# Optimization experiments

Measured on AMD Instinct MI355X. Metric: run time of the kernel, lower is better.

The kernel has to match this reference:

```python
import jax, jax.numpy as jnp
import numpy as np

OUT, IN = 4096, 4096
NNZ = 838860  # 0.05 * OUT * IN
ALPHA = 1.0   # set_privacy(True)


def setup_inputs() -> dict:
    key = jax.random.key(0)
    k1, k2, k3, k4, k5, k6 = jax.random.split(key, 6)
    x = jax.random.normal(k1, (2, 2048, IN), dtype=jnp.float32)
    # packed uint4 pairs stored as bytes (kept in int32 per spec; values in [0,256))
    base_packed = jax.random.randint(k2, (OUT, IN // 2), 0, 256, dtype=jnp.int32)
    # per-row dequant scales (positive, small, like ceiling/7)
    scales = jax.random.uniform(k3, (OUT, 1), dtype=jnp.float32, minval=1e-3, maxval=5e-2)
    ortho_vals = jax.random.normal(k4, (NNZ,), dtype=jnp.float32) * 0.02
    ortho_rows = jax.random.randint(k5, (NNZ,), 0, OUT, dtype=jnp.int32)
    ortho_cols = jax.random.randint(k6, (NNZ,), 0, IN, dtype=jnp.int32)
    return {"x": x, "base_packed": base_packed, "scales": scales,
            "ortho_vals": ortho_vals, "ortho_rows": ortho_rows, "ortho_cols": ortho_cols}


def _dequant(base_packed, scales):
    # unpack two int4 values per byte: col 2k <- low nibble, col 2k+1 <- high nibble
    p = base_packed.astype(jnp.int32)
    low = p & 0xF
    high = (p >> 4) & 0xF
    O, K = p.shape
    w_int4 = jnp.stack([low, high], axis=-1).reshape(O, 2 * K) - 8  # offset-binary -> [-8, 7]
    return w_int4.astype(jnp.float32) * scales  # [O, I]


def reference(x, base_packed, scales, ortho_vals, ortho_rows, ortho_cols):
    O = base_packed.shape[0]
    I = 2 * base_packed.shape[1]
    w_base = _dequant(base_packed, scales)  # [O, I] fp32
    # sparse outlier residual scattered into dense weight (CSR spmm equivalent)
    w_corr = jnp.zeros((O, I), jnp.float32).at[ortho_rows, ortho_cols].add(ortho_vals)
    w = w_base + ALPHA * w_corr
    x_flat = x.reshape(-1, I).astype(jnp.float32)
    out = x_flat @ w.T  # [N, O]
    return out.reshape(x.shape[:-1] + (O,)).astype(x.dtype)
```

## Files before the change

### kernel.cpp

```cpp
#include <hip/hip_runtime.h>
#include <cstdint>
#include <cstddef>

typedef __bf16 bf16x8 __attribute__((ext_vector_type(8)));
typedef float f32x4 __attribute__((ext_vector_type(4)));
typedef unsigned short ushort8 __attribute__((ext_vector_type(8)));

#define OUT_DIM 4096
#define IN_DIM 4096
#define NT 64


__device__ __forceinline__ unsigned short f2bf(float f) {
  unsigned u = __float_as_uint(f);
  return (unsigned short)((u + 0x7FFFu + ((u >> 16) & 1u)) >> 16);
}

__device__ __forceinline__ void async_copy16(const void* g, void* l) {
  __builtin_amdgcn_global_load_lds(
      (const __attribute__((address_space(1))) unsigned int*)g,
      (__attribute__((address_space(3))) unsigned int*)l, 16, 0, 0);
}


__global__ __launch_bounds__(256) void dequant_kernel(
    const int* __restrict__ packed, const float* __restrict__ scales,
    unsigned short* __restrict__ wb) {
  int idx = blockIdx.x * 256 + threadIdx.x;
  int4 p = reinterpret_cast<const int4*>(packed)[idx];
  float s = scales[idx >> 9];
  ushort8 o;
  o[0] = f2bf((float)((p.x & 15) - 8) * s);
  o[1] = f2bf((float)(((p.x >> 4) & 15) - 8) * s);
  o[2] = f2bf((float)((p.y & 15) - 8) * s);
  o[3] = f2bf((float)(((p.y >> 4) & 15) - 8) * s);
  o[4] = f2bf((float)((p.z & 15) - 8) * s);
  o[5] = f2bf((float)(((p.z >> 4) & 15) - 8) * s);
  o[6] = f2bf((float)((p.w & 15) - 8) * s);
  o[7] = f2bf((float)(((p.w >> 4) & 15) - 8) * s);
  *reinterpret_cast<ushort8*>(&wb[(size_t)idx * 8]) = o;
}

__global__ __launch_bounds__(256) void scatter_bf16_kernel(
    const float* __restrict__ vals, const int* __restrict__ rows,
    const int* __restrict__ cols, unsigned short* __restrict__ wb, int nnz) {
  int i = blockIdx.x * 256 + threadIdx.x;
  if (i >= nnz) return;
  size_t idx = (size_t)rows[i] * IN_DIM + cols[i];
  unsigned int* word = (unsigned int*)(wb + (idx & ~(size_t)1));
  const bool hi = (idx & 1) != 0;
  const float v = vals[i];
  unsigned int old = *word, assumed;
  do {
    assumed = old;
    unsigned short h = hi ? (unsigned short)(assumed >> 16)
                          : (unsigned short)(assumed & 0xFFFFu);
    float f = __uint_as_float((unsigned)h << 16);
    unsigned short nh = f2bf(f + v);
    unsigned int nw = hi ? ((assumed & 0x0000FFFFu) | ((unsigned)nh << 16))
                         : ((assumed & 0xFFFF0000u) | (unsigned)nh);
    old = atomicCAS(word, assumed, nw);
  } while (old != assumed);
}

__global__ __launch_bounds__(256) void cvt_kernel(
    const float* __restrict__ in, unsigned short* __restrict__ out) {
  int i = blockIdx.x * 256 + threadIdx.x;
  float4 a = reinterpret_cast<const float4*>(in)[2 * i];
  float4 b = reinterpret_cast<const float4*>(in)[2 * i + 1];
  ushort8 o;
  o[0] = f2bf(a.x); o[1] = f2bf(a.y); o[2] = f2bf(a.z); o[3] = f2bf(a.w);
  o[4] = f2bf(b.x); o[5] = f2bf(b.y); o[6] = f2bf(b.z); o[7] = f2bf(b.w);
  *reinterpret_cast<ushort8*>(&out[(size_t)i * 8]) = o;
}


#define SB(buf, op, kh) ((((buf) * 4) + ((op) * 2) + (kh)) * 16384)

#define STAGE(buf, op, kh, kt)                                              \
  do {                                                                      \
    const unsigned short* gsrc_ =                                           \
        (op) ? (const unsigned short*)((const char*)gA + dBA) : gA;         \
    const unsigned short* g_ = gsrc_ + (kt) * 64 + (kh) * 32;               \
    unsigned short* l_ =                                                    \
        (unsigned short*)((char*)lds + SB(buf, op, kh)) + wave * 512;       \
    async_copy16(g_, l_);                                                   \
    async_copy16(g_ + 128 * IN_DIM, l_ + 4096);                             \
  } while (0)

#define MFMA_ __builtin_amdgcn_mfma_f32_16x16x32_bf16

#define LDA4(d0, d1, d2, d3, BUF, KS, MH)                                   \
  d0 = *(const bf16x8*)(ldsc + (laneA + SB(BUF, 0, KS) + (MH) * 4096 + 0)); \
  d1 = *(const bf16x8*)(ldsc + (laneA + SB(BUF, 0, KS) + (MH) * 4096 + 1024)); \
  d2 = *(const bf16x8*)(ldsc + (laneA + SB(BUF, 0, KS) + (MH) * 4096 + 2048)); \
  d3 = *(const bf16x8*)(ldsc + (laneA + SB(BUF, 0, KS) + (MH) * 4096 + 3072))

#define LDB4(d0, d1, d2, d3, BUF, KS)                                       \
  d0 = *(const bf16x8*)(ldsc + (laneB + SB(BUF, 1, KS) + 0));               \
  d1 = *(const bf16x8*)(ldsc + (laneB + SB(BUF, 1, KS) + 1024));            \
  d2 = *(const bf16x8*)(ldsc + (laneB + SB(BUF, 1, KS) + 2048));            \
  d3 = *(const bf16x8*)(ldsc + (laneB + SB(BUF, 1, KS) + 3072))

#define MM16(MH, A0, A1, A2, A3, B0, B1, B2, B3)                            \
  acc[(MH) * 4 + 0][0] = MFMA_(A0, B0, acc[(MH) * 4 + 0][0], 0, 0, 0);      \
  acc[(MH) * 4 + 0][1] = MFMA_(A0, B1, acc[(MH) * 4 + 0][1], 0, 0, 0);      \
  acc[(MH) * 4 + 0][2] = MFMA_(A0, B2, acc[(MH) * 4 + 0][2], 0, 0, 0);      \
  acc[(MH) * 4 + 0][3] = MFMA_(A0, B3, acc[(MH) * 4 + 0][3], 0, 0, 0);      \
  acc[(MH) * 4 + 1][0] = MFMA_(A1, B0, acc[(MH) * 4 + 1][0], 0, 0, 0);      \
  acc[(MH) * 4 + 1][1] = MFMA_(A1, B1, acc[(MH) * 4 + 1][1], 0, 0, 0);      \
  acc[(MH) * 4 + 1][2] = MFMA_(A1, B2, acc[(MH) * 4 + 1][2], 0, 0, 0);      \
  acc[(MH) * 4 + 1][3] = MFMA_(A1, B3, acc[(MH) * 4 + 1][3], 0, 0, 0);      \
  acc[(MH) * 4 + 2][0] = MFMA_(A2, B0, acc[(MH) * 4 + 2][0], 0, 0, 0);      \
  acc[(MH) * 4 + 2][1] = MFMA_(A2, B1, acc[(MH) * 4 + 2][1], 0, 0, 0);      \
  acc[(MH) * 4 + 2][2] = MFMA_(A2, B2, acc[(MH) * 4 + 2][2], 0, 0, 0);      \
  acc[(MH) * 4 + 2][3] = MFMA_(A2, B3, acc[(MH) * 4 + 2][3], 0, 0, 0);      \
  acc[(MH) * 4 + 3][0] = MFMA_(A3, B0, acc[(MH) * 4 + 3][0], 0, 0, 0);      \
  acc[(MH) * 4 + 3][1] = MFMA_(A3, B1, acc[(MH) * 4 + 3][1], 0, 0, 0);      \
  acc[(MH) * 4 + 3][2] = MFMA_(A3, B2, acc[(MH) * 4 + 3][2], 0, 0, 0);      \
  acc[(MH) * 4 + 3][3] = MFMA_(A3, B3, acc[(MH) * 4 + 3][3], 0, 0, 0)

#define PHASE8(BUF, KS, MH, STAGEST, DOWAIT)                                \
  do {                                                                      \
    bf16x8 a0_, a1_, a2_, a3_;                                              \
    LDA4(a0_, a1_, a2_, a3_, BUF, KS, MH);                                  \
    LDB4(bB0, bB1, bB2, bB3, BUF, KS);                                      \
    STAGEST;                                                                \
    if (DOWAIT) asm volatile("s_waitcnt vmcnt(8)" ::: "memory");            \
    __builtin_amdgcn_s_barrier();                                           \
    asm volatile("s_waitcnt lgkmcnt(0)" ::: "memory");                      \
    __builtin_amdgcn_s_setprio(1);                                          \
    MM16(MH, a0_, a1_, a2_, a3_, bB0, bB1, bB2, bB3);                       \
    __builtin_amdgcn_s_setprio(0);                                          \
    __builtin_amdgcn_s_barrier();                                           \
  } while (0)

#define PHASE4(BUF, KS, MH, STAGEST, DOWAIT)                                \
  do {                                                                      \
    bf16x8 a0_, a1_, a2_, a3_;                                              \
    LDA4(a0_, a1_, a2_, a3_, BUF, KS, MH);                                  \
    STAGEST;                                                                \
    if (DOWAIT) asm volatile("s_waitcnt vmcnt(8)" ::: "memory");            \
    __builtin_amdgcn_s_barrier();                                           \
    asm volatile("s_waitcnt lgkmcnt(0)" ::: "memory");                      \
    __builtin_amdgcn_s_setprio(1);                                          \
    MM16(MH, a0_, a1_, a2_, a3_, bB0, bB1, bB2, bB3);                       \
    __builtin_amdgcn_s_setprio(0);                                          \
    __builtin_amdgcn_s_barrier();                                           \
  } while (0)

#define MINC(x) ((x) < NT ? (x) : (NT - 1))

#define TILE(BUF, t)                                                        \
  do {                                                                      \
    PHASE8(BUF, 0, 0, STAGE(1 - (BUF), 0, 1, MINC((t) + 1)), 0);            \
    PHASE4(BUF, 0, 1, STAGE(1 - (BUF), 1, 1, MINC((t) + 1)), 1);            \
    PHASE8(BUF, 1, 0, STAGE(BUF, 0, 0, MINC((t) + 2)), 0);                  \
    PHASE4(BUF, 1, 1, STAGE(BUF, 1, 0, MINC((t) + 2)), 1);                  \
  } while (0)

__global__ __launch_bounds__(512, 2) void gemm_kernel(
    const unsigned short* __restrict__ A,
    const unsigned short* __restrict__ B,
    float* __restrict__ C) {
  __shared__ __align__(16) unsigned short lds[65536];
  const char* ldsc = (const char*)lds;

  const int bid = blockIdx.x;
  const int xcd = bid & 7, i_ = bid >> 3;
  const int bm = (xcd >> 1) * 4 + (i_ >> 3);
  const int bn = (xcd & 1) * 8 + (i_ & 7);
  const int m0 = bm * 256, n0 = bn * 256;

  const int tid = threadIdx.x;
  const int wave = tid >> 6, lane = tid & 63;
  const int wm = wave >> 2, wn = wave & 3;
  const int lrow = lane & 15, lk = lane >> 4;

  const int r0 = tid >> 2, s0 = tid & 3;
  const int s0s = s0 ^ ((r0 >> 1) & 3);
  const unsigned short* gA = A + (size_t)(m0 + r0) * IN_DIM + s0s * 8;
  const ptrdiff_t dBA = ((const char*)B - (const char*)A) +
                        (ptrdiff_t)(n0 - m0) * IN_DIM * 2;

  const int lks = lk ^ ((lrow >> 1) & 3);
  const int laneA = (wm * 128 + lrow) * 64 + lks * 16;
  const int laneB = (wn * 64 + lrow) * 64 + lks * 16;

  f32x4 acc[8][4];
#pragma unroll
  for (int mi = 0; mi < 8; ++mi)
#pragma unroll
    for (int ni = 0; ni < 4; ++ni) acc[mi][ni] = (f32x4){0.f, 0.f, 0.f, 0.f};

  bf16x8 bB0, bB1, bB2, bB3;

  STAGE(0, 0, 0, 0); STAGE(0, 1, 0, 0);
  asm volatile("" ::: "memory");
  STAGE(0, 0, 1, 0); STAGE(0, 1, 1, 0);
  asm volatile("" ::: "memory");
  STAGE(1, 0, 0, 1); STAGE(1, 1, 0, 1);
  asm volatile("s_waitcnt vmcnt(8)" ::: "memory");
  __builtin_amdgcn_s_barrier();

#pragma unroll 1
  for (int p = 0; p < NT / 2; ++p) {
    const int te = 2 * p;
    TILE(0, te);
    TILE(1, te + 1);
  }
  asm volatile("s_waitcnt vmcnt(0) lgkmcnt(0)" ::: "memory");

#pragma unroll
  for (int mi = 0; mi < 8; ++mi)
#pragma unroll
    for (int ni = 0; ni < 4; ++ni) {
      int m = m0 + wm * 128 + mi * 16 + lk * 4;
      int n = n0 + wn * 64 + ni * 16 + lrow;
      float* cp = &C[(size_t)m * OUT_DIM + n];
#pragma unroll
      for (int r = 0; r < 4; ++r) cp[(size_t)r * OUT_DIM] = acc[mi][ni][r];
    }
}


extern "C" void kernel_launch(void* const* d_in, const int* in_sizes, int n_in,
                              void* d_out, int out_size, void* d_ws, size_t ws_size,
                              hipStream_t stream) {
  const float* x      = (const float*)d_in[0];
  const int*   packed = (const int*)d_in[1];
  const float* scales = (const float*)d_in[2];
  const float* vals   = (const float*)d_in[3];
  const int*   rows   = (const int*)d_in[4];
  const int*   cols   = (const int*)d_in[5];
  float* out = (float*)d_out;

  const int nnz = in_sizes[3];

  char* ws = (char*)d_ws;
  const size_t MB = 1024 * 1024;
  unsigned short* Wb = (unsigned short*)ws;
  unsigned short* Xb = (unsigned short*)(ws + 32 * MB);

  dequant_kernel<<<8192, 256, 0, stream>>>(packed, scales, Wb);
  scatter_bf16_kernel<<<(nnz + 255) / 256, 256, 0, stream>>>(vals, rows, cols, Wb, nnz);
  cvt_kernel<<<8192, 256, 0, stream>>>(x, Xb);
  gemm_kernel<<<256, 512, 0, stream>>>(Xb, Wb, out);
}
```

Before: 185.1 us.

## Fuse prep kernels, use packed bf16 atomics for scatter, reschedule GEMM pipeline

Merges the weight dequantization and activation conversion into one launch. The CAS-loop scatter becomes a hardware global_atomic_pk_add_bf16, with each value rounded to bf16 before it is added. The GEMM main loop is restructured: each phase now loads both k-halves for a quarter of the A tile, B fragments are loaded once per tile, and the staging/wait schedule uses a single buffer-ahead with vmcnt(2). The atomic changes rounding slightly, since the value is converted to bf16 first, and the new pipeline schedule risks exposed load latency.

```diff
diff --git a/kernel.cpp b/kernel.cpp
--- a/kernel.cpp
+++ b/kernel.cpp
@@ -23,55 +23,47 @@
 }
 
 
-__global__ __launch_bounds__(256) void dequant_kernel(
+__global__ __launch_bounds__(256) void prep_kernel(
     const int* __restrict__ packed, const float* __restrict__ scales,
-    unsigned short* __restrict__ wb) {
-  int idx = blockIdx.x * 256 + threadIdx.x;
-  int4 p = reinterpret_cast<const int4*>(packed)[idx];
-  float s = scales[idx >> 9];
-  ushort8 o;
-  o[0] = f2bf((float)((p.x & 15) - 8) * s);
-  o[1] = f2bf((float)(((p.x >> 4) & 15) - 8) * s);
-  o[2] = f2bf((float)((p.y & 15) - 8) * s);
-  o[3] = f2bf((float)(((p.y >> 4) & 15) - 8) * s);
-  o[4] = f2bf((float)((p.z & 15) - 8) * s);
-  o[5] = f2bf((float)(((p.z >> 4) & 15) - 8) * s);
-  o[6] = f2bf((float)((p.w & 15) - 8) * s);
-  o[7] = f2bf((float)(((p.w >> 4) & 15) - 8) * s);
-  *reinterpret_cast<ushort8*>(&wb[(size_t)idx * 8]) = o;
-}
-
-__global__ __launch_bounds__(256) void scatter_bf16_kernel(
+    unsigned short* __restrict__ wb, const float* __restrict__ x,
+    unsigned short* __restrict__ xb) {
+  int b = blockIdx.x;
+  if (b < 8192) {
+    int idx = b * 256 + threadIdx.x;
+    int4 p = reinterpret_cast<const int4*>(packed)[idx];
+    float s = scales[idx >> 9];
+    ushort8 o;
+    o[0] = f2bf((float)((p.x & 15) - 8) * s);
+    o[1] = f2bf((float)(((p.x >> 4) & 15) - 8) * s);
+    o[2] = f2bf((float)((p.y & 15) - 8) * s);
+    o[3] = f2bf((float)(((p.y >> 4) & 15) - 8) * s);
+    o[4] = f2bf((float)((p.z & 15) - 8) * s);
+    o[5] = f2bf((float)(((p.z >> 4) & 15) - 8) * s);
+    o[6] = f2bf((float)((p.w & 15) - 8) * s);
+    o[7] = f2bf((float)(((p.w >> 4) & 15) - 8) * s);
+    *reinterpret_cast<ushort8*>(&wb[(size_t)idx * 8]) = o;
+  } else {
+    int i = (b - 8192) * 256 + threadIdx.x;
+    float4 a = reinterpret_cast<const float4*>(x)[2 * i];
+    float4 c = reinterpret_cast<const float4*>(x)[2 * i + 1];
+    ushort8 o;
+    o[0] = f2bf(a.x); o[1] = f2bf(a.y); o[2] = f2bf(a.z); o[3] = f2bf(a.w);
+    o[4] = f2bf(c.x); o[5] = f2bf(c.y); o[6] = f2bf(c.z); o[7] = f2bf(c.w);
+    *reinterpret_cast<ushort8*>(&xb[(size_t)i * 8]) = o;
+  }
+}
+
+__global__ __launch_bounds__(256) void scatter_pk_kernel(
     const float* __restrict__ vals, const int* __restrict__ rows,
     const int* __restrict__ cols, unsigned short* __restrict__ wb, int nnz) {
   int i = blockIdx.x * 256 + threadIdx.x;
   if (i >= nnz) return;
   size_t idx = (size_t)rows[i] * IN_DIM + cols[i];
   unsigned int* word = (unsigned int*)(wb + (idx & ~(size_t)1));
-  const bool hi = (idx & 1) != 0;
-  const float v = vals[i];
-  unsigned int old = *word, assumed;
-  do {
-    assumed = old;
-    unsigned short h = hi ? (unsigned short)(assumed >> 16)
-                          : (unsigned short)(assumed & 0xFFFFu);
-    float f = __uint_as_float((unsigned)h << 16);
-    unsigned short nh = f2bf(f + v);
-    unsigned int nw = hi ? ((assumed & 0x0000FFFFu) | ((unsigned)nh << 16))
-                         : ((assumed & 0xFFFF0000u) | (unsigned)nh);
-    old = atomicCAS(word, assumed, nw);
-  } while (old != assumed);
-}
-
-__global__ __launch_bounds__(256) void cvt_kernel(
-    const float* __restrict__ in, unsigned short* __restrict__ out) {
-  int i = blockIdx.x * 256 + threadIdx.x;
-  float4 a = reinterpret_cast<const float4*>(in)[2 * i];
-  float4 b = reinterpret_cast<const float4*>(in)[2 * i + 1];
-  ushort8 o;
-  o[0] = f2bf(a.x); o[1] = f2bf(a.y); o[2] = f2bf(a.z); o[3] = f2bf(a.w);
-  o[4] = f2bf(b.x); o[5] = f2bf(b.y); o[6] = f2bf(b.z); o[7] = f2bf(b.w);
-  *reinterpret_cast<ushort8*>(&out[(size_t)i * 8]) = o;
+  unsigned short h = f2bf(vals[i]);
+  unsigned int data = (idx & 1) ? ((unsigned)h << 16) : (unsigned)h;
+  asm volatile("global_atomic_pk_add_bf16 %0, %1, off"
+               :: "v"(word), "v"(data) : "memory");
 }
 
 
@@ -90,11 +82,11 @@
 
 #define MFMA_ __builtin_amdgcn_mfma_f32_16x16x32_bf16
 
-#define LDA4(d0, d1, d2, d3, BUF, KS, MH)                                   \
-  d0 = *(const bf16x8*)(ldsc + (laneA + SB(BUF, 0, KS) + (MH) * 4096 + 0)); \
-  d1 = *(const bf16x8*)(ldsc + (laneA + SB(BUF, 0, KS) + (MH) * 4096 + 1024)); \
-  d2 = *(const bf16x8*)(ldsc + (laneA + SB(BUF, 0, KS) + (MH) * 4096 + 2048)); \
-  d3 = *(const bf16x8*)(ldsc + (laneA + SB(BUF, 0, KS) + (MH) * 4096 + 3072))
+#define LDAQ(BUF, Q)                                                        \
+  a00 = *(const bf16x8*)(ldsc + (laneA + SB(BUF, 0, 0) + (2*(Q)) * 1024));  \
+  a01 = *(const bf16x8*)(ldsc + (laneA + SB(BUF, 0, 0) + (2*(Q)+1) * 1024));\
+  a10 = *(const bf16x8*)(ldsc + (laneA + SB(BUF, 0, 1) + (2*(Q)) * 1024));  \
+  a11 = *(const bf16x8*)(ldsc + (laneA + SB(BUF, 0, 1) + (2*(Q)+1) * 1024))
 
 #define LDB4(d0, d1, d2, d3, BUF, KS)                                       \
   d0 = *(const bf16x8*)(ldsc + (laneB + SB(BUF, 1, KS) + 0));               \
@@ -102,49 +94,47 @@
   d2 = *(const bf16x8*)(ldsc + (laneB + SB(BUF, 1, KS) + 2048));            \
   d3 = *(const bf16x8*)(ldsc + (laneB + SB(BUF, 1, KS) + 3072))
 
-#define MM16(MH, A0, A1, A2, A3, B0, B1, B2, B3)                            \
-  acc[(MH) * 4 + 0][0] = MFMA_(A0, B0, acc[(MH) * 4 + 0][0], 0, 0, 0);      \
-  acc[(MH) * 4 + 0][1] = MFMA_(A0, B1, acc[(MH) * 4 + 0][1], 0, 0, 0);      \
-  acc[(MH) * 4 + 0][2] = MFMA_(A0, B2, acc[(MH) * 4 + 0][2], 0, 0, 0);      \
-  acc[(MH) * 4 + 0][3] = MFMA_(A0, B3, acc[(MH) * 4 + 0][3], 0, 0, 0);      \
-  acc[(MH) * 4 + 1][0] = MFMA_(A1, B0, acc[(MH) * 4 + 1][0], 0, 0, 0);      \
-  acc[(MH) * 4 + 1][1] = MFMA_(A1, B1, acc[(MH) * 4 + 1][1], 0, 0, 0);      \
-  acc[(MH) * 4 + 1][2] = MFMA_(A1, B2, acc[(MH) * 4 + 1][2], 0, 0, 0);      \
-  acc[(MH) * 4 + 1][3] = MFMA_(A1, B3, acc[(MH) * 4 + 1][3], 0, 0, 0);      \
-  acc[(MH) * 4 + 2][0] = MFMA_(A2, B0, acc[(MH) * 4 + 2][0], 0, 0, 0);      \
-  acc[(MH) * 4 + 2][1] = MFMA_(A2, B1, acc[(MH) * 4 + 2][1], 0, 0, 0);      \
-  acc[(MH) * 4 + 2][2] = MFMA_(A2, B2, acc[(MH) * 4 + 2][2], 0, 0, 0);      \
-  acc[(MH) * 4 + 2][3] = MFMA_(A2, B3, acc[(MH) * 4 + 2][3], 0, 0, 0);      \
-  acc[(MH) * 4 + 3][0] = MFMA_(A3, B0, acc[(MH) * 4 + 3][0], 0, 0, 0);      \
-  acc[(MH) * 4 + 3][1] = MFMA_(A3, B1, acc[(MH) * 4 + 3][1], 0, 0, 0);      \
-  acc[(MH) * 4 + 3][2] = MFMA_(A3, B2, acc[(MH) * 4 + 3][2], 0, 0, 0);      \
-  acc[(MH) * 4 + 3][3] = MFMA_(A3, B3, acc[(MH) * 4 + 3][3], 0, 0, 0)
-
-#define PHASE8(BUF, KS, MH, STAGEST, DOWAIT)                                \
-  do {                                                                      \
-    bf16x8 a0_, a1_, a2_, a3_;                                              \
-    LDA4(a0_, a1_, a2_, a3_, BUF, KS, MH);                                  \
-    LDB4(bB0, bB1, bB2, bB3, BUF, KS);                                      \
-    STAGEST;                                                                \
-    if (DOWAIT) asm volatile("s_waitcnt vmcnt(8)" ::: "memory");            \
-    __builtin_amdgcn_s_barrier();                                           \
+#define MMQ(Q)                                                              \
+  acc[2*(Q)+0][0] = MFMA_(a00, b00, acc[2*(Q)+0][0], 0, 0, 0);              \
+  acc[2*(Q)+0][1] = MFMA_(a00, b01, acc[2*(Q)+0][1], 0, 0, 0);              \
+  acc[2*(Q)+0][2] = MFMA_(a00, b02, acc[2*(Q)+0][2], 0, 0, 0);              \
+  acc[2*(Q)+0][3] = MFMA_(a00, b03, acc[2*(Q)+0][3], 0, 0, 0);              \
+  acc[2*(Q)+1][0] = MFMA_(a01, b00, acc[2*(Q)+1][0], 0, 0, 0);              \
+  acc[2*(Q)+1][1] = MFMA_(a01, b01, acc[2*(Q)+1][1], 0, 0, 0);              \
+  acc[2*(Q)+1][2] = MFMA_(a01, b02, acc[2*(Q)+1][2], 0, 0, 0);              \
+  acc[2*(Q)+1][3] = MFMA_(a01, b03, acc[2*(Q)+1][3], 0, 0, 0);              \
+  acc[2*(Q)+0][0] = MFMA_(a10, b10, acc[2*(Q)+0][0], 0, 0, 0);              \
+  acc[2*(Q)+0][1] = MFMA_(a10, b11, acc[2*(Q)+0][1], 0, 0, 0);              \
+  acc[2*(Q)+0][2] = MFMA_(a10, b12, acc[2*(Q)+0][2], 0, 0, 0);              \
+  acc[2*(Q)+0][3] = MFMA_(a10, b13, acc[2*(Q)+0][3], 0, 0, 0);              \
+  acc[2*(Q)+1][0] = MFMA_(a11, b10, acc[2*(Q)+1][0], 0, 0, 0);              \
+  acc[2*(Q)+1][1] = MFMA_(a11, b11, acc[2*(Q)+1][1], 0, 0, 0);              \
+  acc[2*(Q)+1][2] = MFMA_(a11, b12, acc[2*(Q)+1][2], 0, 0, 0);              \
+  acc[2*(Q)+1][3] = MFMA_(a11, b13, acc[2*(Q)+1][3], 0, 0, 0)
+
+#define PH1(BUF, tS)                                                        \
+  do {                                                                      \
+    STAGE(1 - (BUF), 1, 0, tS);                                             \
+    asm volatile("s_waitcnt vmcnt(2)" ::: "memory");                        \
+    __builtin_amdgcn_s_barrier();                                           \
+    LDB4(b00, b01, b02, b03, BUF, 0);                                       \
+    LDB4(b10, b11, b12, b13, BUF, 1);                                       \
+    LDAQ(BUF, 0);                                                           \
     asm volatile("s_waitcnt lgkmcnt(0)" ::: "memory");                      \
     __builtin_amdgcn_s_setprio(1);                                          \
-    MM16(MH, a0_, a1_, a2_, a3_, bB0, bB1, bB2, bB3);                       \
+    MMQ(0);                                                                 \
     __builtin_amdgcn_s_setprio(0);                                          \
     __builtin_amdgcn_s_barrier();                                           \
   } while (0)
 
-#define PHASE4(BUF, KS, MH, STAGEST, DOWAIT)                                \
-  do {                                                                      \
-    bf16x8 a0_, a1_, a2_, a3_;                                              \
-    LDA4(a0_, a1_, a2_, a3_, BUF, KS, MH);                                  \
-    STAGEST;                                                                \
-    if (DOWAIT) asm volatile("s_waitcnt vmcnt(8)" ::: "memory");            \
+#define PHQ(BUF, Q, OP, KH, tS)                                             \
+  do {                                                                      \
+    LDAQ(BUF, Q);                                                           \
+    STAGE(1 - (BUF), OP, KH, tS);                                           \
     __builtin_amdgcn_s_barrier();                                           \
     asm volatile("s_waitcnt lgkmcnt(0)" ::: "memory");                      \
     __builtin_amdgcn_s_setprio(1);                                          \
-    MM16(MH, a0_, a1_, a2_, a3_, bB0, bB1, bB2, bB3);                       \
+    MMQ(Q);                                                                 \
     __builtin_amdgcn_s_setprio(0);                                          \
     __builtin_amdgcn_s_barrier();                                           \
   } while (0)
@@ -153,10 +143,10 @@
 
 #define TILE(BUF, t)                                                        \
   do {                                                                      \
-    PHASE8(BUF, 0, 0, STAGE(1 - (BUF), 0, 1, MINC((t) + 1)), 0);            \
-    PHASE4(BUF, 0, 1, STAGE(1 - (BUF), 1, 1, MINC((t) + 1)), 1);            \
-    PHASE8(BUF, 1, 0, STAGE(BUF, 0, 0, MINC((t) + 2)), 0);                  \
-    PHASE4(BUF, 1, 1, STAGE(BUF, 1, 0, MINC((t) + 2)), 1);                  \
+    PH1(BUF, MINC((t) + 1));                                                \
+    PHQ(BUF, 1, 1, 1, MINC((t) + 1));                                       \
+    PHQ(BUF, 2, 0, 0, MINC((t) + 1));                                       \
+    PHQ(BUF, 3, 0, 1, MINC((t) + 1));                                       \
   } while (0)
 
 __global__ __launch_bounds__(512, 2) void gemm_kernel(
@@ -193,21 +183,21 @@
 #pragma unroll
     for (int ni = 0; ni < 4; ++ni) acc[mi][ni] = (f32x4){0.f, 0.f, 0.f, 0.f};
 
-  bf16x8 bB0, bB1, bB2, bB3;
-
-  STAGE(0, 0, 0, 0); STAGE(0, 1, 0, 0);
+  bf16x8 b00, b01, b02, b03, b10, b11, b12, b13;
+  bf16x8 a00, a01, a10, a11;
+
+  STAGE(0, 1, 0, 0);
   asm volatile("" ::: "memory");
-  STAGE(0, 0, 1, 0); STAGE(0, 1, 1, 0);
+  STAGE(0, 1, 1, 0);
   asm volatile("" ::: "memory");
-  STAGE(1, 0, 0, 1); STAGE(1, 1, 0, 1);
-  asm volatile("s_waitcnt vmcnt(8)" ::: "memory");
-  __builtin_amdgcn_s_barrier();
+  STAGE(0, 0, 0, 0);
+  asm volatile("" ::: "memory");
+  STAGE(0, 0, 1, 0);
 
 #pragma unroll 1
   for (int p = 0; p < NT / 2; ++p) {
-    const int te = 2 * p;
-    TILE(0, te);
-    TILE(1, te + 1);
+    TILE(0, 2 * p);
+    TILE(1, 2 * p + 1);
   }
   asm volatile("s_waitcnt vmcnt(0) lgkmcnt(0)" ::: "memory");
 
@@ -242,8 +232,7 @@
   unsigned short* Wb = (unsigned short*)ws;
   unsigned short* Xb = (unsigned short*)(ws + 32 * MB);
 
-  dequant_kernel<<<8192, 256, 0, stream>>>(packed, scales, Wb);
-  scatter_bf16_kernel<<<(nnz + 255) / 256, 256, 0, stream>>>(vals, rows, cols, Wb, nnz);
-  cvt_kernel<<<8192, 256, 0, stream>>>(x, Xb);
+  prep_kernel<<<16384, 256, 0, stream>>>(packed, scales, Wb, x, Xb);
+  scatter_pk_kernel<<<(nnz + 255) / 256, 256, 0, stream>>>(vals, rows, cols, Wb, nnz);
   gemm_kernel<<<256, 512, 0, stream>>>(Xb, Wb, out);
 }
```

Result: no change. 182.7 us, median of 4 (-1.3%).
